# Kernel tuning notes

Measured on AMD Instinct MI355X. Metric: run time of the kernel, lower is better.

The kernel has to match this reference:

```python
import jax, jax.numpy as jnp
import numpy as np

IGNORE_LABEL = 255
THRESH = 0.9
MIN_KEPT = 10000


def setup_inputs() -> dict:
    key = jax.random.key(0)
    k1, k2 = jax.random.split(key)
    n, c, d, h, w = 2, 12, 64, 128, 128
    predict = jax.random.normal(k1, (n, c, d, h, w), dtype=jnp.float32)
    target = jax.random.randint(k2, (n, d, h, w), 0, c, dtype=jnp.int64)
    return {"predict": predict, "target": target}


def reference(predict, target):
    n, c, d, h, w = predict.shape
    # rollaxis(predict, 1).reshape(c, -1): class-major flattening, matching target.ravel()
    logits = jnp.moveaxis(predict, 1, 0).reshape(c, -1)          # (c, N)
    labels = target.reshape(-1)                                   # (N,)
    valid = labels != IGNORE_LABEL
    safe_lab = jnp.where(valid, labels, 0)

    logp = jax.nn.log_softmax(logits, axis=0)                     # (c, N), stable softmax
    lp_at_label = jnp.take_along_axis(logp, safe_lab[None, :], axis=0)[0]  # (N,)
    prob_at_label = jnp.exp(lp_at_label)                          # softmax prob of true class

    num_valid = valid.sum()
    # k-th smallest true-class prob among valid pixels (invalid -> +inf pushed to end)
    sorted_prob = jnp.sort(jnp.where(valid, prob_at_label, jnp.inf))
    k_idx = jnp.maximum(jnp.minimum(MIN_KEPT, num_valid) - 1, 0)
    th_val = sorted_prob[k_idx]
    threshold = jnp.maximum(th_val, THRESH)

    # if min_kept >= num_valid: keep all valid; else keep hard examples (prob <= threshold)
    keep_all = MIN_KEPT >= num_valid
    kept = valid & jnp.where(keep_all, True, prob_at_label <= threshold)

    # masked mean cross-entropy (CrossEntropyLoss with ignore_index, mean reduction)
    nll = -lp_at_label
    num = jnp.sum(jnp.where(kept, nll, 0.0))
    cnt = jnp.sum(kept)
    loss = num / jnp.maximum(cnt, 1).astype(nll.dtype)
    return loss
```

## Files before the change

### kernel.cpp

```cpp
#include <hip/hip_runtime.h>
#include <hip/hip_bf16.h>
#include <math.h>


#define IGNORE_LABEL 255
#define MIN_KEPT 10000u

constexpr int   C         = 12;
constexpr int   PIX_SHIFT = 20;
constexpr int   NBINS     = 2048;
constexpr float BIN_SCALE = (float)NBINS / 0.1f;

struct Ws {
    double       sum_p3;
    unsigned int cnt_p3;
    unsigned int flag;
    float        threshold;
    unsigned int pad[11];
    unsigned int hist[NBINS];
};

__device__ inline float wave_reduce_f(float v) {
    #pragma unroll
    for (int o = 32; o > 0; o >>= 1) v += __shfl_down(v, o, 64);
    return v;
}
__device__ inline unsigned int wave_reduce_u(unsigned int v) {
    #pragma unroll
    for (int o = 32; o > 0; o >>= 1) v += __shfl_down(v, o, 64);
    return v;
}
__device__ inline double wave_reduce_d(double v) {
    #pragma unroll
    for (int o = 32; o > 0; o >>= 1) v += __shfl_down(v, o, 64);
    return v;
}

__device__ inline void compute4(const float* __restrict__ pred,
                                const int* __restrict__ tgt, int t,
                                float prob[4], float nll[4], bool valid[4]) {
    const int p0  = t << 2;
    const int ni  = p0 >> PIX_SHIFT;
    const int rem = p0 & ((1 << PIX_SHIFT) - 1);
    const float* base = pred + (((size_t)ni * C) << PIX_SHIFT) + rem;

    const int4 li = *(const int4*)(tgt + p0);
    int lab[4] = {li.x, li.y, li.z, li.w};

    float s[4]     = {0.0f, 0.0f, 0.0f, 0.0f};
    float l_lab[4] = {0.0f, 0.0f, 0.0f, 0.0f};

    #pragma unroll
    for (int ci = 0; ci < C; ++ci) {
        const float4 v = *(const float4*)(base + ((size_t)ci << PIX_SHIFT));
        const float vv[4] = {v.x, v.y, v.z, v.w};
        #pragma unroll
        for (int j = 0; j < 4; ++j) {
            s[j] += __expf(vv[j]);
            if (lab[j] == ci) l_lab[j] = vv[j];
        }
    }
    #pragma unroll
    for (int j = 0; j < 4; ++j) {
        const float ls = __logf(s[j]);
        nll[j]   = ls - l_lab[j];
        prob[j]  = __expf(l_lab[j] - ls);
        valid[j] = (lab[j] != IGNORE_LABEL);
    }
}

__global__ __launch_bounds__(256) void main_pass_kernel(
        const float* __restrict__ pred, const int* __restrict__ tgt,
        Ws* __restrict__ ws, uint4* __restrict__ partials, int npix_q) {
    const int t = blockIdx.x * blockDim.x + threadIdx.x;

    float        my_sle = 0.0f, my_sva = 0.0f;
    unsigned int my_cle = 0u,   my_cva = 0u;

    if (t < npix_q) {
        float prob[4], nll[4]; bool valid[4];
        compute4(pred, tgt, t, prob, nll, valid);
        #pragma unroll
        for (int j = 0; j < 4; ++j) {
            if (valid[j]) {
                my_cva += 1u;
                my_sva += nll[j];
                if (prob[j] <= 0.9f) {
                    my_cle += 1u;
                    my_sle += nll[j];
                } else {
                    int b = (int)((prob[j] - 0.9f) * BIN_SCALE);
                    b = b < 0 ? 0 : (b >= NBINS - 1 ? NBINS - 1 : b);
                    atomicAdd(&ws->hist[b], 1u);
                }
            }
        }
    }

    __shared__ float        s_le[4], s_va[4];
    __shared__ unsigned int s_cle[4], s_cva[4];
    const int wid = threadIdx.x >> 6, lane = threadIdx.x & 63;
    const float        r_le = wave_reduce_f(my_sle);
    const float        r_va = wave_reduce_f(my_sva);
    const unsigned int r_cl = wave_reduce_u(my_cle);
    const unsigned int r_cv = wave_reduce_u(my_cva);
    if (lane == 0) { s_le[wid] = r_le; s_va[wid] = r_va; s_cle[wid] = r_cl; s_cva[wid] = r_cv; }
    __syncthreads();
    if (threadIdx.x == 0) {
        uint4 p;
        p.x = __float_as_uint(s_le[0] + s_le[1] + s_le[2] + s_le[3]);
        p.y = __float_as_uint(s_va[0] + s_va[1] + s_va[2] + s_va[3]);
        p.z = s_cle[0] + s_cle[1] + s_cle[2] + s_cle[3];
        p.w = s_cva[0] + s_cva[1] + s_cva[2] + s_cva[3];
        partials[blockIdx.x] = p;
    }
}

__global__ __launch_bounds__(1024) void reduce_finalize_kernel(
        Ws* __restrict__ ws, const uint4* __restrict__ partials,
        int nblocks, float* __restrict__ out) {
    double       sle = 0.0, sva = 0.0;
    unsigned int cle = 0u,  cva = 0u;
    for (int i = threadIdx.x; i < nblocks; i += 1024) {
        const uint4 p = partials[i];
        sle += (double)__uint_as_float(p.x);
        sva += (double)__uint_as_float(p.y);
        cle += p.z;
        cva += p.w;
    }
    __shared__ double       d_le[16], d_va[16];
    __shared__ unsigned int u_le[16], u_va[16];
    const int wid = threadIdx.x >> 6, lane = threadIdx.x & 63;
    const double       r_sle = wave_reduce_d(sle);
    const double       r_sva = wave_reduce_d(sva);
    const unsigned int r_cle = wave_reduce_u(cle);
    const unsigned int r_cva = wave_reduce_u(cva);
    if (lane == 0) { d_le[wid] = r_sle; d_va[wid] = r_sva; u_le[wid] = r_cle; u_va[wid] = r_cva; }
    __syncthreads();
    if (threadIdx.x == 0) {
        double       t_sle = 0.0, t_sva = 0.0;
        unsigned int t_cle = 0u,  t_cva = 0u;
        #pragma unroll
        for (int i = 0; i < 16; ++i) {
            t_sle += d_le[i]; t_sva += d_va[i]; t_cle += u_le[i]; t_cva += u_va[i];
        }
        const unsigned int nv = t_cva;
        const unsigned int k  = nv < MIN_KEPT ? nv : MIN_KEPT;
        if (MIN_KEPT >= nv) {
            out[0] = (float)(t_sva / (double)(nv > 0u ? nv : 1u));
            ws->flag = 0u;
        } else if (t_cle >= k) {
            out[0] = (float)(t_sle / (double)(t_cle > 0u ? t_cle : 1u));
            ws->flag = 0u;
        } else {
            unsigned int cum = t_cle;
            int b = NBINS - 1;
            for (int i = 0; i < NBINS; ++i) {
                cum += ws->hist[i];
                if (cum >= k) { b = i; break; }
            }
            ws->threshold = 0.9f + (float)(b + 1) * (0.1f / (float)NBINS);
            ws->flag = 1u;
            out[0] = 0.0f;
        }
    }
}

__global__ __launch_bounds__(256) void fallback_pass_kernel(
        const float* __restrict__ pred, const int* __restrict__ tgt,
        Ws* __restrict__ ws, int npix_q) {
    if (ws->flag == 0u) return;
    const float th = ws->threshold;
    const int stride = gridDim.x * blockDim.x;

    float        my_s = 0.0f;
    unsigned int my_c = 0u;
    for (int t = blockIdx.x * blockDim.x + threadIdx.x; t < npix_q; t += stride) {
        float prob[4], nll[4]; bool valid[4];
        compute4(pred, tgt, t, prob, nll, valid);
        #pragma unroll
        for (int j = 0; j < 4; ++j) {
            if (valid[j] && prob[j] <= th) { my_c += 1u; my_s += nll[j]; }
        }
    }
    __shared__ float        s_s[4];
    __shared__ unsigned int s_c[4];
    const int wid = threadIdx.x >> 6, lane = threadIdx.x & 63;
    const float        r_s = wave_reduce_f(my_s);
    const unsigned int r_c = wave_reduce_u(my_c);
    if (lane == 0) { s_s[wid] = r_s; s_c[wid] = r_c; }
    __syncthreads();
    if (threadIdx.x == 0) {
        float        t_s = s_s[0] + s_s[1] + s_s[2] + s_s[3];
        unsigned int t_c = s_c[0] + s_c[1] + s_c[2] + s_c[3];
        if (t_s != 0.0f) atomicAdd(&ws->sum_p3, (double)t_s);
        if (t_c)         atomicAdd(&ws->cnt_p3, t_c);
    }
}

__global__ void fallback_finalize_kernel(Ws* __restrict__ ws, float* __restrict__ out) {
    if (ws->flag) {
        const unsigned int cnt = ws->cnt_p3;
        out[0] = (float)(ws->sum_p3 / (double)(cnt > 0u ? cnt : 1u));
    }
}

extern "C" void kernel_launch(void* const* d_in, const int* in_sizes, int n_in,
                              void* d_out, int out_size, void* d_ws, size_t ws_size,
                              hipStream_t stream) {
    const float* pred = (const float*)d_in[0];
    const int*   tgt  = (const int*)d_in[1];
    float*       out  = (float*)d_out;
    Ws*          ws   = (Ws*)d_ws;
    uint4*       partials = (uint4*)((char*)d_ws + sizeof(Ws));

    const int npix   = in_sizes[1];
    const int npix_q = npix >> 2;
    const int blocks = (npix_q + 255) / 256;

    hipMemsetAsync(d_ws, 0, sizeof(Ws), stream);
    main_pass_kernel<<<blocks, 256, 0, stream>>>(pred, tgt, ws, partials, npix_q);
    reduce_finalize_kernel<<<1, 1024, 0, stream>>>(ws, partials, blocks, out);
    fallback_pass_kernel<<<512, 256, 0, stream>>>(pred, tgt, ws, npix_q);
    fallback_finalize_kernel<<<1, 1, 0, stream>>>(ws, out);
}
```

Measured before the change: 162.6 us.

## Process two pixel quads per thread and fold fallback finalize into pass kernel

The main pass now has each thread handle two float4 pixel groups, one grid-stride apart, so each thread keeps more independent loads in flight. The grid is halved and launch bounds ask for higher occupancy. The separate fallback finalize kernel is removed: the last block of the fallback pass, found through an atomic done counter, writes the result, saving one launch. The fallback grid also shrinks to 128 blocks, which slows that path whenever it actually runs.

```diff
diff --git a/kernel.cpp b/kernel.cpp
--- a/kernel.cpp
+++ b/kernel.cpp
@@ -8,6 +8,7 @@
 
 constexpr int   C         = 12;
 constexpr int   PIX_SHIFT = 20;
+constexpr int   PIX_MASK  = (1 << PIX_SHIFT) - 1;
 constexpr int   NBINS     = 2048;
 constexpr float BIN_SCALE = (float)NBINS / 0.1f;
 
@@ -16,7 +17,8 @@
     unsigned int cnt_p3;
     unsigned int flag;
     float        threshold;
-    unsigned int pad[11];
+    unsigned int done;
+    unsigned int pad[10];
     unsigned int hist[NBINS];
 };
 
@@ -38,18 +40,15 @@
 
 __device__ inline void compute4(const float* __restrict__ pred,
                                 const int* __restrict__ tgt, int t,
-                                float prob[4], float nll[4], bool valid[4]) {
-    const int p0  = t << 2;
-    const int ni  = p0 >> PIX_SHIFT;
-    const int rem = p0 & ((1 << PIX_SHIFT) - 1);
-    const float* base = pred + (((size_t)ni * C) << PIX_SHIFT) + rem;
-
+                                float prob[4], float nll[4], int lab[4]) {
+    const int p0 = t << 2;
+    const float* base = pred +
+        (((size_t)(p0 >> PIX_SHIFT) * C) << PIX_SHIFT) + (p0 & PIX_MASK);
     const int4 li = *(const int4*)(tgt + p0);
-    int lab[4] = {li.x, li.y, li.z, li.w};
+    lab[0] = li.x; lab[1] = li.y; lab[2] = li.z; lab[3] = li.w;
 
     float s[4]     = {0.0f, 0.0f, 0.0f, 0.0f};
     float l_lab[4] = {0.0f, 0.0f, 0.0f, 0.0f};
-
     #pragma unroll
     for (int ci = 0; ci < C; ++ci) {
         const float4 v = *(const float4*)(base + ((size_t)ci << PIX_SHIFT));
@@ -63,38 +62,87 @@
     #pragma unroll
     for (int j = 0; j < 4; ++j) {
         const float ls = __logf(s[j]);
-        nll[j]   = ls - l_lab[j];
-        prob[j]  = __expf(l_lab[j] - ls);
-        valid[j] = (lab[j] != IGNORE_LABEL);
-    }
-}
-
-__global__ __launch_bounds__(256) void main_pass_kernel(
+        nll[j]  = ls - l_lab[j];
+        prob[j] = __expf(l_lab[j] - ls);
+    }
+}
+
+__device__ inline void compute4x2(const float* __restrict__ pred,
+                                  const int* __restrict__ tgt, int ta, int tb,
+                                  float prob[8], float nll[8], int lab[8]) {
+    const int pa = ta << 2, pb = tb << 2;
+    const float* ba = pred +
+        (((size_t)(pa >> PIX_SHIFT) * C) << PIX_SHIFT) + (pa & PIX_MASK);
+    const float* bb = pred +
+        (((size_t)(pb >> PIX_SHIFT) * C) << PIX_SHIFT) + (pb & PIX_MASK);
+    const int4 la = *(const int4*)(tgt + pa);
+    const int4 lb = *(const int4*)(tgt + pb);
+    lab[0] = la.x; lab[1] = la.y; lab[2] = la.z; lab[3] = la.w;
+    lab[4] = lb.x; lab[5] = lb.y; lab[6] = lb.z; lab[7] = lb.w;
+
+    float s[8]     = {0,0,0,0,0,0,0,0};
+    float l_lab[8] = {0,0,0,0,0,0,0,0};
+    #pragma unroll
+    for (int ci = 0; ci < C; ++ci) {
+        const float4 va = *(const float4*)(ba + ((size_t)ci << PIX_SHIFT));
+        const float4 vb = *(const float4*)(bb + ((size_t)ci << PIX_SHIFT));
+        const float vv[8] = {va.x, va.y, va.z, va.w, vb.x, vb.y, vb.z, vb.w};
+        #pragma unroll
+        for (int j = 0; j < 8; ++j) {
+            s[j] += __expf(vv[j]);
+            if (lab[j] == ci) l_lab[j] = vv[j];
+        }
+    }
+    #pragma unroll
+    for (int j = 0; j < 8; ++j) {
+        const float ls = __logf(s[j]);
+        nll[j]  = ls - l_lab[j];
+        prob[j] = __expf(l_lab[j] - ls);
+    }
+}
+
+__device__ inline void accum_pixel(float prob, float nll, int lab,
+                                   Ws* __restrict__ ws,
+                                   float& sle, float& sva,
+                                   unsigned int& cle, unsigned int& cva) {
+    if (lab != IGNORE_LABEL) {
+        cva += 1u;
+        sva += nll;
+        if (prob <= 0.9f) {
+            cle += 1u;
+            sle += nll;
+        } else {
+            int b = (int)((prob - 0.9f) * BIN_SCALE);
+            b = b < 0 ? 0 : (b >= NBINS - 1 ? NBINS - 1 : b);
+            atomicAdd(&ws->hist[b], 1u);
+        }
+    }
+}
+
+__global__ __launch_bounds__(256, 4) void main_pass_kernel(
         const float* __restrict__ pred, const int* __restrict__ tgt,
         Ws* __restrict__ ws, uint4* __restrict__ partials, int npix_q) {
-    const int t = blockIdx.x * blockDim.x + threadIdx.x;
+    const int nthreads = gridDim.x * blockDim.x;
+    const int tid = blockIdx.x * blockDim.x + threadIdx.x;
 
     float        my_sle = 0.0f, my_sva = 0.0f;
     unsigned int my_cle = 0u,   my_cva = 0u;
 
+    int t = tid;
+    while (t + nthreads < npix_q) {
+        float prob[8], nll[8]; int lab[8];
+        compute4x2(pred, tgt, t, t + nthreads, prob, nll, lab);
+        #pragma unroll
+        for (int j = 0; j < 8; ++j)
+            accum_pixel(prob[j], nll[j], lab[j], ws, my_sle, my_sva, my_cle, my_cva);
+        t += 2 * nthreads;
+    }
     if (t < npix_q) {
-        float prob[4], nll[4]; bool valid[4];
-        compute4(pred, tgt, t, prob, nll, valid);
-        #pragma unroll
-        for (int j = 0; j < 4; ++j) {
-            if (valid[j]) {
-                my_cva += 1u;
-                my_sva += nll[j];
-                if (prob[j] <= 0.9f) {
-                    my_cle += 1u;
-                    my_sle += nll[j];
-                } else {
-                    int b = (int)((prob[j] - 0.9f) * BIN_SCALE);
-                    b = b < 0 ? 0 : (b >= NBINS - 1 ? NBINS - 1 : b);
-                    atomicAdd(&ws->hist[b], 1u);
-                }
-            }
-        }
+        float prob[4], nll[4]; int lab[4];
+        compute4(pred, tgt, t, prob, nll, lab);
+        #pragma unroll
+        for (int j = 0; j < 4; ++j)
+            accum_pixel(prob[j], nll[j], lab[j], ws, my_sle, my_sva, my_cle, my_cva);
     }
 
     __shared__ float        s_le[4], s_va[4];
@@ -166,9 +214,9 @@
     }
 }
 
-__global__ __launch_bounds__(256) void fallback_pass_kernel(
+__global__ __launch_bounds__(256) void fallback_kernel(
         const float* __restrict__ pred, const int* __restrict__ tgt,
-        Ws* __restrict__ ws, int npix_q) {
+        Ws* __restrict__ ws, float* __restrict__ out, int npix_q) {
     if (ws->flag == 0u) return;
     const float th = ws->threshold;
     const int stride = gridDim.x * blockDim.x;
@@ -176,11 +224,11 @@
     float        my_s = 0.0f;
     unsigned int my_c = 0u;
     for (int t = blockIdx.x * blockDim.x + threadIdx.x; t < npix_q; t += stride) {
-        float prob[4], nll[4]; bool valid[4];
-        compute4(pred, tgt, t, prob, nll, valid);
+        float prob[4], nll[4]; int lab[4];
+        compute4(pred, tgt, t, prob, nll, lab);
         #pragma unroll
         for (int j = 0; j < 4; ++j) {
-            if (valid[j] && prob[j] <= th) { my_c += 1u; my_s += nll[j]; }
+            if (lab[j] != IGNORE_LABEL && prob[j] <= th) { my_c += 1u; my_s += nll[j]; }
         }
     }
     __shared__ float        s_s[4];
@@ -191,17 +239,16 @@
     if (lane == 0) { s_s[wid] = r_s; s_c[wid] = r_c; }
     __syncthreads();
     if (threadIdx.x == 0) {
-        float        t_s = s_s[0] + s_s[1] + s_s[2] + s_s[3];
-        unsigned int t_c = s_c[0] + s_c[1] + s_c[2] + s_c[3];
+        const float        t_s = s_s[0] + s_s[1] + s_s[2] + s_s[3];
+        const unsigned int t_c = s_c[0] + s_c[1] + s_c[2] + s_c[3];
         if (t_s != 0.0f) atomicAdd(&ws->sum_p3, (double)t_s);
         if (t_c)         atomicAdd(&ws->cnt_p3, t_c);
-    }
-}
-
-__global__ void fallback_finalize_kernel(Ws* __restrict__ ws, float* __restrict__ out) {
-    if (ws->flag) {
-        const unsigned int cnt = ws->cnt_p3;
-        out[0] = (float)(ws->sum_p3 / (double)(cnt > 0u ? cnt : 1u));
+        __threadfence();
+        const unsigned int prev = atomicAdd(&ws->done, 1u);
+        if (prev == gridDim.x - 1u) {
+            const unsigned int cnt = ws->cnt_p3;
+            out[0] = (float)(ws->sum_p3 / (double)(cnt > 0u ? cnt : 1u));
+        }
     }
 }
 
@@ -216,11 +263,10 @@
 
     const int npix   = in_sizes[1];
     const int npix_q = npix >> 2;
-    const int blocks = (npix_q + 255) / 256;
+    const int blocks = (npix_q + 511) / 512;
 
     hipMemsetAsync(d_ws, 0, sizeof(Ws), stream);
     main_pass_kernel<<<blocks, 256, 0, stream>>>(pred, tgt, ws, partials, npix_q);
     reduce_finalize_kernel<<<1, 1024, 0, stream>>>(ws, partials, blocks, out);
-    fallback_pass_kernel<<<512, 256, 0, stream>>>(pred, tgt, ws, npix_q);
-    fallback_finalize_kernel<<<1, 1, 0, stream>>>(ws, out);
-}
+    fallback_kernel<<<128, 256, 0, stream>>>(pred, tgt, ws, out, npix_q);
+}
```

Measured after the change: 161.5 us. No clear change (-0.7%).

## Fuse reduction and finalize kernels via last-block-done atomic counters

Applied to the files above, without the earlier changes.

Folds the single-block reduce/finalize kernel into the main pass: each block writes its partial, bumps an atomic counter, and the last block to finish does the global reduction and threshold selection. The fallback finalize is merged the same way into the fallback kernel. This cuts the launch count from four to two. Main-pass blocks grow from 256 to 1024 threads, and the fallback grid shrinks to 128 blocks. The trade-off is extra fences and atomics, plus a serial tail in the last block.

```diff
diff --git a/kernel.cpp b/kernel.cpp
--- a/kernel.cpp
+++ b/kernel.cpp
@@ -8,6 +8,7 @@
 
 constexpr int   C         = 12;
 constexpr int   PIX_SHIFT = 20;
+constexpr int   PIX_MASK  = (1 << PIX_SHIFT) - 1;
 constexpr int   NBINS     = 2048;
 constexpr float BIN_SCALE = (float)NBINS / 0.1f;
 
@@ -16,7 +17,9 @@
     unsigned int cnt_p3;
     unsigned int flag;
     float        threshold;
-    unsigned int pad[11];
+    unsigned int done;
+    unsigned int done2;
+    unsigned int pad[9];
     unsigned int hist[NBINS];
 };
 
@@ -30,26 +33,18 @@
     for (int o = 32; o > 0; o >>= 1) v += __shfl_down(v, o, 64);
     return v;
 }
-__device__ inline double wave_reduce_d(double v) {
-    #pragma unroll
-    for (int o = 32; o > 0; o >>= 1) v += __shfl_down(v, o, 64);
-    return v;
-}
 
 __device__ inline void compute4(const float* __restrict__ pred,
                                 const int* __restrict__ tgt, int t,
-                                float prob[4], float nll[4], bool valid[4]) {
-    const int p0  = t << 2;
-    const int ni  = p0 >> PIX_SHIFT;
-    const int rem = p0 & ((1 << PIX_SHIFT) - 1);
-    const float* base = pred + (((size_t)ni * C) << PIX_SHIFT) + rem;
-
+                                float prob[4], float nll[4], int lab[4]) {
+    const int p0 = t << 2;
+    const float* base = pred +
+        (((size_t)(p0 >> PIX_SHIFT) * C) << PIX_SHIFT) + (p0 & PIX_MASK);
     const int4 li = *(const int4*)(tgt + p0);
-    int lab[4] = {li.x, li.y, li.z, li.w};
+    lab[0] = li.x; lab[1] = li.y; lab[2] = li.z; lab[3] = li.w;
 
     float s[4]     = {0.0f, 0.0f, 0.0f, 0.0f};
     float l_lab[4] = {0.0f, 0.0f, 0.0f, 0.0f};
-
     #pragma unroll
     for (int ci = 0; ci < C; ++ci) {
         const float4 v = *(const float4*)(base + ((size_t)ci << PIX_SHIFT));
@@ -63,26 +58,26 @@
     #pragma unroll
     for (int j = 0; j < 4; ++j) {
         const float ls = __logf(s[j]);
-        nll[j]   = ls - l_lab[j];
-        prob[j]  = __expf(l_lab[j] - ls);
-        valid[j] = (lab[j] != IGNORE_LABEL);
-    }
-}
-
-__global__ __launch_bounds__(256) void main_pass_kernel(
+        nll[j]  = ls - l_lab[j];
+        prob[j] = __expf(l_lab[j] - ls);
+    }
+}
+
+__global__ __launch_bounds__(1024, 8) void main_pass_kernel(
         const float* __restrict__ pred, const int* __restrict__ tgt,
-        Ws* __restrict__ ws, uint4* __restrict__ partials, int npix_q) {
-    const int t = blockIdx.x * blockDim.x + threadIdx.x;
+        Ws* __restrict__ ws, uint4* __restrict__ partials,
+        float* __restrict__ out, int npix_q) {
+    const int tid = blockIdx.x * blockDim.x + threadIdx.x;
 
     float        my_sle = 0.0f, my_sva = 0.0f;
     unsigned int my_cle = 0u,   my_cva = 0u;
 
-    if (t < npix_q) {
-        float prob[4], nll[4]; bool valid[4];
-        compute4(pred, tgt, t, prob, nll, valid);
+    if (tid < npix_q) {
+        float prob[4], nll[4]; int lab[4];
+        compute4(pred, tgt, tid, prob, nll, lab);
         #pragma unroll
         for (int j = 0; j < 4; ++j) {
-            if (valid[j]) {
+            if (lab[j] != IGNORE_LABEL) {
                 my_cva += 1u;
                 my_sva += nll[j];
                 if (prob[j] <= 0.9f) {
@@ -97,8 +92,9 @@
         }
     }
 
-    __shared__ float        s_le[4], s_va[4];
-    __shared__ unsigned int s_cle[4], s_cva[4];
+    __shared__ float        s_le[16], s_va[16];
+    __shared__ unsigned int s_cle[16], s_cva[16];
+    __shared__ int          s_last;
     const int wid = threadIdx.x >> 6, lane = threadIdx.x & 63;
     const float        r_le = wave_reduce_f(my_sle);
     const float        r_va = wave_reduce_f(my_sva);
@@ -107,42 +103,51 @@
     if (lane == 0) { s_le[wid] = r_le; s_va[wid] = r_va; s_cle[wid] = r_cl; s_cva[wid] = r_cv; }
     __syncthreads();
     if (threadIdx.x == 0) {
+        float        t_le = 0.0f, t_va = 0.0f;
+        unsigned int t_cl = 0u,   t_cv = 0u;
+        #pragma unroll
+        for (int i = 0; i < 16; ++i) {
+            t_le += s_le[i]; t_va += s_va[i]; t_cl += s_cle[i]; t_cv += s_cva[i];
+        }
         uint4 p;
-        p.x = __float_as_uint(s_le[0] + s_le[1] + s_le[2] + s_le[3]);
-        p.y = __float_as_uint(s_va[0] + s_va[1] + s_va[2] + s_va[3]);
-        p.z = s_cle[0] + s_cle[1] + s_cle[2] + s_cle[3];
-        p.w = s_cva[0] + s_cva[1] + s_cva[2] + s_cva[3];
+        p.x = __float_as_uint(t_le);
+        p.y = __float_as_uint(t_va);
+        p.z = t_cl;
+        p.w = t_cv;
         partials[blockIdx.x] = p;
-    }
-}
-
-__global__ __launch_bounds__(1024) void reduce_finalize_kernel(
-        Ws* __restrict__ ws, const uint4* __restrict__ partials,
-        int nblocks, float* __restrict__ out) {
+        __threadfence();
+        const unsigned int prev = atomicAdd(&ws->done, 1u);
+        s_last = (prev == gridDim.x - 1u);
+    }
+    __syncthreads();
+    if (!s_last) return;
+
+    __threadfence();
     double       sle = 0.0, sva = 0.0;
     unsigned int cle = 0u,  cva = 0u;
-    for (int i = threadIdx.x; i < nblocks; i += 1024) {
+    for (int i = threadIdx.x; i < gridDim.x; i += blockDim.x) {
         const uint4 p = partials[i];
         sle += (double)__uint_as_float(p.x);
         sva += (double)__uint_as_float(p.y);
         cle += p.z;
         cva += p.w;
     }
-    __shared__ double       d_le[16], d_va[16];
-    __shared__ unsigned int u_le[16], u_va[16];
-    const int wid = threadIdx.x >> 6, lane = threadIdx.x & 63;
-    const double       r_sle = wave_reduce_d(sle);
-    const double       r_sva = wave_reduce_d(sva);
-    const unsigned int r_cle = wave_reduce_u(cle);
-    const unsigned int r_cva = wave_reduce_u(cva);
-    if (lane == 0) { d_le[wid] = r_sle; d_va[wid] = r_sva; u_le[wid] = r_cle; u_va[wid] = r_cva; }
+    __shared__ double d_le[16], d_va[16];
+    {
+        double rs = sle, rv = sva;
+        #pragma unroll
+        for (int o = 32; o > 0; o >>= 1) { rs += __shfl_down(rs, o, 64); rv += __shfl_down(rv, o, 64); }
+        const unsigned int rcl = wave_reduce_u(cle);
+        const unsigned int rcv = wave_reduce_u(cva);
+        if (lane == 0) { d_le[wid] = rs; d_va[wid] = rv; s_cle[wid] = rcl; s_cva[wid] = rcv; }
+    }
     __syncthreads();
     if (threadIdx.x == 0) {
         double       t_sle = 0.0, t_sva = 0.0;
         unsigned int t_cle = 0u,  t_cva = 0u;
         #pragma unroll
         for (int i = 0; i < 16; ++i) {
-            t_sle += d_le[i]; t_sva += d_va[i]; t_cle += u_le[i]; t_cva += u_va[i];
+            t_sle += d_le[i]; t_sva += d_va[i]; t_cle += s_cle[i]; t_cva += s_cva[i];
         }
         const unsigned int nv = t_cva;
         const unsigned int k  = nv < MIN_KEPT ? nv : MIN_KEPT;
@@ -160,15 +165,16 @@
                 if (cum >= k) { b = i; break; }
             }
             ws->threshold = 0.9f + (float)(b + 1) * (0.1f / (float)NBINS);
+            __threadfence();
             ws->flag = 1u;
             out[0] = 0.0f;
         }
     }
 }
 
-__global__ __launch_bounds__(256) void fallback_pass_kernel(
+__global__ __launch_bounds__(256) void fallback_kernel(
         const float* __restrict__ pred, const int* __restrict__ tgt,
-        Ws* __restrict__ ws, int npix_q) {
+        Ws* __restrict__ ws, float* __restrict__ out, int npix_q) {
     if (ws->flag == 0u) return;
     const float th = ws->threshold;
     const int stride = gridDim.x * blockDim.x;
@@ -176,11 +182,11 @@
     float        my_s = 0.0f;
     unsigned int my_c = 0u;
     for (int t = blockIdx.x * blockDim.x + threadIdx.x; t < npix_q; t += stride) {
-        float prob[4], nll[4]; bool valid[4];
-        compute4(pred, tgt, t, prob, nll, valid);
+        float prob[4], nll[4]; int lab[4];
+        compute4(pred, tgt, t, prob, nll, lab);
         #pragma unroll
         for (int j = 0; j < 4; ++j) {
-            if (valid[j] && prob[j] <= th) { my_c += 1u; my_s += nll[j]; }
+            if (lab[j] != IGNORE_LABEL && prob[j] <= th) { my_c += 1u; my_s += nll[j]; }
         }
     }
     __shared__ float        s_s[4];
@@ -191,17 +197,16 @@
     if (lane == 0) { s_s[wid] = r_s; s_c[wid] = r_c; }
     __syncthreads();
     if (threadIdx.x == 0) {
-        float        t_s = s_s[0] + s_s[1] + s_s[2] + s_s[3];
-        unsigned int t_c = s_c[0] + s_c[1] + s_c[2] + s_c[3];
+        const float        t_s = s_s[0] + s_s[1] + s_s[2] + s_s[3];
+        const unsigned int t_c = s_c[0] + s_c[1] + s_c[2] + s_c[3];
         if (t_s != 0.0f) atomicAdd(&ws->sum_p3, (double)t_s);
         if (t_c)         atomicAdd(&ws->cnt_p3, t_c);
-    }
-}
-
-__global__ void fallback_finalize_kernel(Ws* __restrict__ ws, float* __restrict__ out) {
-    if (ws->flag) {
-        const unsigned int cnt = ws->cnt_p3;
-        out[0] = (float)(ws->sum_p3 / (double)(cnt > 0u ? cnt : 1u));
+        __threadfence();
+        const unsigned int prev = atomicAdd(&ws->done2, 1u);
+        if (prev == gridDim.x - 1u) {
+            const unsigned int cnt = ws->cnt_p3;
+            out[0] = (float)(ws->sum_p3 / (double)(cnt > 0u ? cnt : 1u));
+        }
     }
 }
 
@@ -216,11 +221,9 @@
 
     const int npix   = in_sizes[1];
     const int npix_q = npix >> 2;
-    const int blocks = (npix_q + 255) / 256;
+    const int blocks = (npix_q + 1023) / 1024;
 
     hipMemsetAsync(d_ws, 0, sizeof(Ws), stream);
-    main_pass_kernel<<<blocks, 256, 0, stream>>>(pred, tgt, ws, partials, npix_q);
-    reduce_finalize_kernel<<<1, 1024, 0, stream>>>(ws, partials, blocks, out);
-    fallback_pass_kernel<<<512, 256, 0, stream>>>(pred, tgt, ws, npix_q);
-    fallback_finalize_kernel<<<1, 1, 0, stream>>>(ws, out);
-}
+    main_pass_kernel<<<blocks, 1024, 0, stream>>>(pred, tgt, ws, partials, out, npix_q);
+    fallback_kernel<<<128, 256, 0, stream>>>(pred, tgt, ws, out, npix_q);
+}
```

After: 175.4 us. +7.9%, slower.

## Process eight pixels per thread and fold fallback finalize into last block

Applied to the files above, without the earlier changes.

The main pass now has each thread handle eight pixels using two float4 loads per class, halving the block count and the partials to reduce, and adds a launch-bounds occupancy hint. The separate fallback finalize kernel is removed; the last fallback block, found through an atomic done counter, writes the output, saving one kernel launch. The fallback grid is also shrunk to 128 blocks. Per-thread register use rises and there are fewer threads to hide memory latency.

```diff
diff --git a/kernel.cpp b/kernel.cpp
--- a/kernel.cpp
+++ b/kernel.cpp
@@ -8,6 +8,7 @@
 
 constexpr int   C         = 12;
 constexpr int   PIX_SHIFT = 20;
+constexpr int   PIX_MASK  = (1 << PIX_SHIFT) - 1;
 constexpr int   NBINS     = 2048;
 constexpr float BIN_SCALE = (float)NBINS / 0.1f;
 
@@ -16,7 +17,9 @@
     unsigned int cnt_p3;
     unsigned int flag;
     float        threshold;
-    unsigned int pad[11];
+    unsigned int done;
+    unsigned int done2;
+    unsigned int pad[9];
     unsigned int hist[NBINS];
 };
 
@@ -36,60 +39,49 @@
     return v;
 }
 
-__device__ inline void compute4(const float* __restrict__ pred,
-                                const int* __restrict__ tgt, int t,
-                                float prob[4], float nll[4], bool valid[4]) {
-    const int p0  = t << 2;
-    const int ni  = p0 >> PIX_SHIFT;
-    const int rem = p0 & ((1 << PIX_SHIFT) - 1);
-    const float* base = pred + (((size_t)ni * C) << PIX_SHIFT) + rem;
-
-    const int4 li = *(const int4*)(tgt + p0);
-    int lab[4] = {li.x, li.y, li.z, li.w};
-
-    float s[4]     = {0.0f, 0.0f, 0.0f, 0.0f};
-    float l_lab[4] = {0.0f, 0.0f, 0.0f, 0.0f};
-
-    #pragma unroll
-    for (int ci = 0; ci < C; ++ci) {
-        const float4 v = *(const float4*)(base + ((size_t)ci << PIX_SHIFT));
-        const float vv[4] = {v.x, v.y, v.z, v.w};
-        #pragma unroll
-        for (int j = 0; j < 4; ++j) {
-            s[j] += __expf(vv[j]);
-            if (lab[j] == ci) l_lab[j] = vv[j];
-        }
-    }
-    #pragma unroll
-    for (int j = 0; j < 4; ++j) {
-        const float ls = __logf(s[j]);
-        nll[j]   = ls - l_lab[j];
-        prob[j]  = __expf(l_lab[j] - ls);
-        valid[j] = (lab[j] != IGNORE_LABEL);
-    }
-}
-
-__global__ __launch_bounds__(256) void main_pass_kernel(
+__global__ __launch_bounds__(256, 4) void main_pass_kernel(
         const float* __restrict__ pred, const int* __restrict__ tgt,
-        Ws* __restrict__ ws, uint4* __restrict__ partials, int npix_q) {
-    const int t = blockIdx.x * blockDim.x + threadIdx.x;
+        Ws* __restrict__ ws, uint4* __restrict__ partials, int npix) {
+    const int tid = blockIdx.x * blockDim.x + threadIdx.x;
 
     float        my_sle = 0.0f, my_sva = 0.0f;
     unsigned int my_cle = 0u,   my_cva = 0u;
 
-    if (t < npix_q) {
-        float prob[4], nll[4]; bool valid[4];
-        compute4(pred, tgt, t, prob, nll, valid);
-        #pragma unroll
-        for (int j = 0; j < 4; ++j) {
-            if (valid[j]) {
+    const int p0 = tid << 3;
+    if (p0 < npix) {
+        const float* base = pred +
+            (((size_t)(p0 >> PIX_SHIFT) * C) << PIX_SHIFT) + (p0 & PIX_MASK);
+        const int4 la = *(const int4*)(tgt + p0);
+        const int4 lb = *(const int4*)(tgt + p0 + 4);
+        const int lab[8] = {la.x, la.y, la.z, la.w, lb.x, lb.y, lb.z, lb.w};
+
+        float E[8]  = {0,0,0,0,0,0,0,0};
+        float ll[8] = {0,0,0,0,0,0,0,0};
+        #pragma unroll
+        for (int ci = 0; ci < C; ++ci) {
+            const float* csrc = base + ((size_t)ci << PIX_SHIFT);
+            const float4 v0 = *(const float4*)(csrc);
+            const float4 v1 = *(const float4*)(csrc + 4);
+            const float vv[8] = {v0.x, v0.y, v0.z, v0.w, v1.x, v1.y, v1.z, v1.w};
+            #pragma unroll
+            for (int j = 0; j < 8; ++j) {
+                E[j] += __expf(vv[j]);
+                if (lab[j] == ci) ll[j] = vv[j];
+            }
+        }
+        #pragma unroll
+        for (int j = 0; j < 8; ++j) {
+            const float ls   = __logf(E[j]);
+            const float nll  = ls - ll[j];
+            const float prob = __expf(ll[j] - ls);
+            if (lab[j] != IGNORE_LABEL) {
                 my_cva += 1u;
-                my_sva += nll[j];
-                if (prob[j] <= 0.9f) {
+                my_sva += nll;
+                if (prob <= 0.9f) {
                     my_cle += 1u;
-                    my_sle += nll[j];
+                    my_sle += nll;
                 } else {
-                    int b = (int)((prob[j] - 0.9f) * BIN_SCALE);
+                    int b = (int)((prob - 0.9f) * BIN_SCALE);
                     b = b < 0 ? 0 : (b >= NBINS - 1 ? NBINS - 1 : b);
                     atomicAdd(&ws->hist[b], 1u);
                 }
@@ -166,9 +158,9 @@
     }
 }
 
-__global__ __launch_bounds__(256) void fallback_pass_kernel(
+__global__ __launch_bounds__(256) void fallback_kernel(
         const float* __restrict__ pred, const int* __restrict__ tgt,
-        Ws* __restrict__ ws, int npix_q) {
+        Ws* __restrict__ ws, float* __restrict__ out, int npix_q) {
     if (ws->flag == 0u) return;
     const float th = ws->threshold;
     const int stride = gridDim.x * blockDim.x;
@@ -176,11 +168,28 @@
     float        my_s = 0.0f;
     unsigned int my_c = 0u;
     for (int t = blockIdx.x * blockDim.x + threadIdx.x; t < npix_q; t += stride) {
-        float prob[4], nll[4]; bool valid[4];
-        compute4(pred, tgt, t, prob, nll, valid);
+        const int p0 = t << 2;
+        const float* base = pred +
+            (((size_t)(p0 >> PIX_SHIFT) * C) << PIX_SHIFT) + (p0 & PIX_MASK);
+        const int4 li = *(const int4*)(tgt + p0);
+        const int lab[4] = {li.x, li.y, li.z, li.w};
+        float s[4] = {0,0,0,0}, l_lab[4] = {0,0,0,0};
+        #pragma unroll
+        for (int ci = 0; ci < C; ++ci) {
+            const float4 v = *(const float4*)(base + ((size_t)ci << PIX_SHIFT));
+            const float vv[4] = {v.x, v.y, v.z, v.w};
+            #pragma unroll
+            for (int j = 0; j < 4; ++j) {
+                s[j] += __expf(vv[j]);
+                if (lab[j] == ci) l_lab[j] = vv[j];
+            }
+        }
         #pragma unroll
         for (int j = 0; j < 4; ++j) {
-            if (valid[j] && prob[j] <= th) { my_c += 1u; my_s += nll[j]; }
+            const float ls   = __logf(s[j]);
+            const float nll  = ls - l_lab[j];
+            const float prob = __expf(l_lab[j] - ls);
+            if (lab[j] != IGNORE_LABEL && prob <= th) { my_c += 1u; my_s += nll; }
         }
     }
     __shared__ float        s_s[4];
@@ -191,17 +200,16 @@
     if (lane == 0) { s_s[wid] = r_s; s_c[wid] = r_c; }
     __syncthreads();
     if (threadIdx.x == 0) {
-        float        t_s = s_s[0] + s_s[1] + s_s[2] + s_s[3];
-        unsigned int t_c = s_c[0] + s_c[1] + s_c[2] + s_c[3];
+        const float        t_s = s_s[0] + s_s[1] + s_s[2] + s_s[3];
+        const unsigned int t_c = s_c[0] + s_c[1] + s_c[2] + s_c[3];
         if (t_s != 0.0f) atomicAdd(&ws->sum_p3, (double)t_s);
         if (t_c)         atomicAdd(&ws->cnt_p3, t_c);
-    }
-}
-
-__global__ void fallback_finalize_kernel(Ws* __restrict__ ws, float* __restrict__ out) {
-    if (ws->flag) {
-        const unsigned int cnt = ws->cnt_p3;
-        out[0] = (float)(ws->sum_p3 / (double)(cnt > 0u ? cnt : 1u));
+        __threadfence();
+        const unsigned int prev = atomicAdd(&ws->done2, 1u);
+        if (prev == gridDim.x - 1u) {
+            const unsigned int cnt = ws->cnt_p3;
+            out[0] = (float)(ws->sum_p3 / (double)(cnt > 0u ? cnt : 1u));
+        }
     }
 }
 
@@ -216,11 +224,10 @@
 
     const int npix   = in_sizes[1];
     const int npix_q = npix >> 2;
-    const int blocks = (npix_q + 255) / 256;
+    const int blocks = (npix / 8 + 255) / 256;
 
     hipMemsetAsync(d_ws, 0, sizeof(Ws), stream);
-    main_pass_kernel<<<blocks, 256, 0, stream>>>(pred, tgt, ws, partials, npix_q);
+    main_pass_kernel<<<blocks, 256, 0, stream>>>(pred, tgt, ws, partials, npix);
     reduce_finalize_kernel<<<1, 1024, 0, stream>>>(ws, partials, blocks, out);
-    fallback_pass_kernel<<<512, 256, 0, stream>>>(pred, tgt, ws, npix_q);
-    fallback_finalize_kernel<<<1, 1, 0, stream>>>(ws, out);
-}
+    fallback_kernel<<<128, 256, 0, stream>>>(pred, tgt, ws, out, npix_q);
+}
```

Result: faster. 157.9 us (-2.9%).
